# Kernel tuning notes

Measured on AMD Instinct MI355X. Metric: run time of the kernel, lower is better.

The kernel has to match this reference:

```python
import jax, jax.numpy as jnp
import numpy as np

KERNEL_MUL = 2.0
KERNEL_NUM = 5


def _pairwise_sq_dists(total):
    # ||a-b||^2 = ||a||^2 + ||b||^2 - 2 a.b  (same math as expand-subtract-square-sum)
    sq = jnp.sum(total * total, axis=1)  # [N]
    gram = total @ total.T               # [N, N]
    d2 = sq[:, None] + sq[None, :] - 2.0 * gram
    return jnp.maximum(d2, 0.0)


def setup_inputs() -> dict:
    key = jax.random.key(0)
    k1, k2 = jax.random.split(key)
    source = jax.random.normal(k1, (4096, 256), dtype=jnp.float32)
    target = jax.random.normal(k2, (4096, 256), dtype=jnp.float32)
    return {"source": source, "target": target}


def reference(source, target):
    bs = source.shape[0]
    n_samples = source.shape[0] + target.shape[0]
    total = jnp.concatenate([source, target], axis=0)  # [N, D]
    l2 = _pairwise_sq_dists(total)                      # [N, N]
    # bandwidth computed from detached distances (torch .data)
    bandwidth = jax.lax.stop_gradient(jnp.sum(l2)) / (n_samples ** 2 - n_samples)
    bandwidth = bandwidth / (KERNEL_MUL ** (KERNEL_NUM // 2))
    kernels = jnp.zeros_like(l2)
    for i in range(KERNEL_NUM):
        kernels = kernels + jnp.exp(-l2 / (bandwidth * (KERNEL_MUL ** i)))
    xx = jnp.mean(kernels[:bs, :bs])
    yy = jnp.mean(kernels[bs:, bs:])
    xy = jnp.mean(kernels[:bs, bs:])
    yx = jnp.mean(kernels[bs:, :bs])
    return xx + yy - xy - yx
```

## Files before the change

kernel.cpp:

```cpp
#include <hip/hip_runtime.h>
#include <stdint.h>
#include <stddef.h>


#define N_TOT 8192
#define D_DIM 256
#define BS    4096
#define NB    64
#define NTILE 2080

typedef float  f32x4  __attribute__((ext_vector_type(4)));
typedef short  bf16x8 __attribute__((ext_vector_type(8)));

typedef __attribute__((address_space(1))) const unsigned int gas_u32;
typedef __attribute__((address_space(3))) unsigned int       lds_u32;

__device__ __forceinline__ unsigned short f2bf(float f) {
  unsigned u = __float_as_uint(f);
  u += 0x7fffu + ((u >> 16) & 1u);
  return (unsigned short)(u >> 16);
}
__device__ __forceinline__ float bf2f(unsigned short s) {
  return __uint_as_float(((unsigned)s) << 16);
}

__global__ void prep_kernel(const float* __restrict__ src, const float* __restrict__ tgt,
                            unsigned short* __restrict__ Xbt, float* __restrict__ sq,
                            float* __restrict__ csp) {
  int tid  = threadIdx.x;
  int w    = tid >> 6, lane = tid & 63;
  int blk  = blockIdx.x;
  float4 cacc = {0.f, 0.f, 0.f, 0.f};

  #pragma unroll
  for (int r = 0; r < 4; ++r) {
    int row = blk * 32 + w * 4 + r;
    const float* rowp = (row < BS) ? (src + (size_t)row * D_DIM)
                                   : (tgt + (size_t)(row - BS) * D_DIM);
    float4 v = reinterpret_cast<const float4*>(rowp)[lane];
    cacc.x += v.x; cacc.y += v.y; cacc.z += v.z; cacc.w += v.w;
    ushort4 b;
    b.x = f2bf(v.x); b.y = f2bf(v.y); b.z = f2bf(v.z); b.w = f2bf(v.w);
    int k = lane * 4;
    size_t off = ((size_t)(row >> 4)) * 4096 + (size_t)(k >> 3) * 128
               + (size_t)((row & 15) * 8) + (k & 7);
    *reinterpret_cast<ushort4*>(Xbt + off) = b;
    float fx = bf2f(b.x), fy = bf2f(b.y), fz = bf2f(b.z), fw = bf2f(b.w);
    float s = fx * fx + fy * fy + fz * fz + fw * fw;
    #pragma unroll
    for (int o = 32; o; o >>= 1) s += __shfl_down(s, o, 64);
    if (lane == 0) sq[row] = s;
  }

  __shared__ float cs[8][256];
  reinterpret_cast<float4*>(&cs[w][0])[lane] = cacc;
  __syncthreads();
  if (tid < 256) {
    float s = 0.f;
    #pragma unroll
    for (int ww = 0; ww < 8; ++ww) s += cs[ww][tid];
    csp[blk * 256 + tid] = s;
  }
}

__global__ void bw_kernel(const float* __restrict__ sq, const float* __restrict__ csp,
                          float* __restrict__ coef) {
  int t = threadIdx.x, w = t >> 6, lane = t & 63;
  double s1 = 0.0;
  #pragma unroll
  for (int i = 0; i < 32; ++i) s1 += (double)sq[t + i * 256];
  double c = 0.0;
  #pragma unroll 16
  for (int b = 0; b < 256; ++b) c += (double)csp[b * 256 + t];
  double s2 = c * c;
  #pragma unroll
  for (int o = 32; o; o >>= 1) { s1 += __shfl_down(s1, o, 64); s2 += __shfl_down(s2, o, 64); }
  __shared__ double rs[4], rs2[4];
  if (lane == 0) { rs[w] = s1; rs2[w] = s2; }
  __syncthreads();
  if (t == 0) {
    double S1 = rs[0] + rs[1] + rs[2] + rs[3];
    double S2 = rs2[0] + rs2[1] + rs2[2] + rs2[3];
    double S  = 2.0 * (double)N_TOT * S1 - 2.0 * S2;
    double bw = (S / ((double)N_TOT * (double)N_TOT - (double)N_TOT)) / 4.0;
    *coef = (float)(-1.4426950408889634 / (16.0 * bw));
  }
}

__launch_bounds__(256, 2)
__global__ void gram_kernel(const unsigned short* __restrict__ Xbt, const float* __restrict__ sq,
                            const float* __restrict__ coefp, double* __restrict__ partial) {
  __shared__ __align__(16) unsigned char Alds[65536];

  int tid = threadIdx.x;
  int w = tid >> 6, lane = tid & 63;
  const int lo = lane & 15, hi = lane >> 4;
  const int wr = w >> 1, wc = w & 1;

  int orig = (int)blockIdx.x;
  int id   = (orig & 7) * (NTILE / 8) + (orig >> 3);

  int bi = 0, bj = 0;
  {
    int rem = id, Mi = 0, Mj = 0;
    for (Mi = 0; Mi < 8; ++Mi) {
      bool found = false;
      for (Mj = Mi; Mj < 8; ++Mj) {
        int cntm = (Mi == Mj) ? 36 : 64;
        if (rem < cntm) { found = true; break; }
        rem -= cntm;
      }
      if (found) break;
    }
    int ti, tj;
    if (Mi == Mj) {
      ti = 0;
      while (rem >= 8 - ti) { rem -= 8 - ti; ++ti; }
      tj = ti + rem;
    } else {
      ti = rem >> 3; tj = rem & 7;
    }
    bi = Mi * 8 + ti; bj = Mj * 8 + tj;
  }

  float factor = ((bi < 32) == (bj < 32)) ? 1.f : -1.f;
  if (bi != bj) factor *= 2.f;

  const char* Xb = (const char*)Xbt;

  {
    const char* srcA = Xb + (size_t)bi * 65536 + w * 16384 + lane * 16;
    unsigned char* dstA = Alds + w * 16384;
    #pragma unroll
    for (int i = 0; i < 16; ++i)
      __builtin_amdgcn_global_load_lds((gas_u32*)(srcA + i * 1024),
                                       (lds_u32*)(dstA + i * 1024), 16, 0, 0);
  }

  const char* pB = Xb + (size_t)(bj * 8 + wc * 4) * 8192 + (hi * 256 + lo * 16);
  const char* pAl = (const char*)Alds + (size_t)(wr * 4) * 8192 + (hi * 256 + lo * 16);

  f32x4 acc[4][4];
  #pragma unroll
  for (int m = 0; m < 4; ++m)
    #pragma unroll
    for (int n = 0; n < 4; ++n) acc[m][n] = (f32x4){0.f, 0.f, 0.f, 0.f};

  __syncthreads();

  #pragma unroll
  for (int kc = 0; kc < 8; ++kc) {
    bf16x8 a[4], b[4];
    #pragma unroll
    for (int n = 0; n < 4; ++n) b[n] = *(const bf16x8*)(pB + n * 8192 + kc * 1024);
    #pragma unroll
    for (int m = 0; m < 4; ++m) a[m] = *(const bf16x8*)(pAl + m * 8192 + kc * 1024);
    #pragma unroll
    for (int m = 0; m < 4; ++m)
      #pragma unroll
      for (int n = 0; n < 4; ++n)
        acc[m][n] = __builtin_amdgcn_mfma_f32_16x16x32_bf16(a[m], b[n], acc[m][n], 0, 0, 0);
  }

  float coef = *coefp;
  float sqj[4], sqi[4][4];
  #pragma unroll
  for (int n = 0; n < 4; ++n) sqj[n] = sq[bj * 128 + wc * 64 + n * 16 + lo];
  #pragma unroll
  for (int m = 0; m < 4; ++m)
    #pragma unroll
    for (int r = 0; r < 4; ++r) sqi[m][r] = sq[bi * 128 + wr * 64 + m * 16 + hi * 4 + r];

  float psum = 0.f;
  #pragma unroll
  for (int m = 0; m < 4; ++m) {
    #pragma unroll
    for (int n = 0; n < 4; ++n) {
      #pragma unroll
      for (int r = 0; r < 4; ++r) {
        float g  = acc[m][n][r];
        float d2 = fmaxf(fmaf(-2.f, g, sqi[m][r] + sqj[n]), 0.f);
        float u  = __builtin_amdgcn_exp2f(d2 * coef);
        float u2 = u * u, u4 = u2 * u2, u8 = u4 * u4, u16 = u8 * u8;
        psum += (u + u2) + (u4 + u8) + u16;
      }
    }
  }
  #pragma unroll
  for (int o = 32; o; o >>= 1) psum += __shfl_down(psum, o, 64);
  __shared__ float wred[4];
  if (lane == 0) wred[w] = psum;
  __syncthreads();
  if (tid == 0)
    partial[id] = (double)((wred[0] + wred[1] + wred[2] + wred[3]) * factor);
}

__global__ void reduce_kernel(const double* __restrict__ partial, float* __restrict__ out) {
  int t = threadIdx.x, w = t >> 6, lane = t & 63;
  double s = 0.0;
  for (int i = t; i < NTILE; i += 256) s += partial[i];
  #pragma unroll
  for (int o = 32; o; o >>= 1) s += __shfl_down(s, o, 64);
  __shared__ double rs[4];
  if (lane == 0) rs[w] = s;
  __syncthreads();
  if (t == 0)
    out[0] = (float)((rs[0] + rs[1] + rs[2] + rs[3]) / ((double)BS * (double)BS));
}

extern "C" void kernel_launch(void* const* d_in, const int* in_sizes, int n_in,
                              void* d_out, int out_size, void* d_ws, size_t ws_size,
                              hipStream_t stream) {
  const float* src = (const float*)d_in[0];
  const float* tgt = (const float*)d_in[1];
  char* ws = (char*)d_ws;
  float*  coef    = (float*)(ws + 0);
  double* partial = (double*)(ws + 64);
  float*  csp     = (float*)(ws + 16704);
  float*  sq      = (float*)(ws + 278848);
  unsigned short* Xbt = (unsigned short*)(ws + 311616);
  float* out = (float*)d_out;

  prep_kernel<<<256, 512, 0, stream>>>(src, tgt, Xbt, sq, csp);
  bw_kernel<<<1, 256, 0, stream>>>(sq, csp, coef);
  gram_kernel<<<NTILE, 256, 0, stream>>>(Xbt, sq, coef, partial);
  reduce_kernel<<<1, 256, 0, stream>>>(partial, out);
}
```

Baseline: 58.77 us.

## Process four consecutive upper-triangle tiles per block, reusing staged A rows

Each gram block now walks four consecutive tiles in row-major upper-triangle order instead of one tile from a blocked 8x8 super-tile ordering. The LDS copy of the A row block is restaged only when the tile row changes, so most tiles skip the 64KB global-to-LDS load. The goal is less A staging traffic and fewer block launches. The cost is a 4x smaller grid (520 blocks), which limits parallelism and latency hiding, and a loss of the previous L2-friendly super-tile ordering for B reads.

```diff
diff --git a/kernel.cpp b/kernel.cpp
--- a/kernel.cpp
+++ b/kernel.cpp
@@ -8,6 +8,7 @@
 #define BS    4096
 #define NB    64
 #define NTILE 2080
+#define NBLK  520
 
 typedef float  f32x4  __attribute__((ext_vector_type(4)));
 typedef short  bf16x8 __attribute__((ext_vector_type(8)));
@@ -98,107 +99,99 @@
   const int wr = w >> 1, wc = w & 1;
 
   int orig = (int)blockIdx.x;
-  int id   = (orig & 7) * (NTILE / 8) + (orig >> 3);
-
-  int bi = 0, bj = 0;
-  {
-    int rem = id, Mi = 0, Mj = 0;
-    for (Mi = 0; Mi < 8; ++Mi) {
-      bool found = false;
-      for (Mj = Mi; Mj < 8; ++Mj) {
-        int cntm = (Mi == Mj) ? 36 : 64;
-        if (rem < cntm) { found = true; break; }
-        rem -= cntm;
-      }
-      if (found) break;
+  int blk  = (orig & 7) * (NBLK / 8) + (orig >> 3);
+  int id   = blk * 4;
+
+  int bi = 0, rem = id;
+  while (rem >= NB - bi) { rem -= NB - bi; ++bi; }
+  int bj = bi + rem;
+
+  const char* Xb = (const char*)Xbt;
+  float coef = *coefp;
+  int bi_staged = -1;
+  double dsum = 0.0;
+
+  for (int t = 0; t < 4; ++t) {
+    if (bi != bi_staged) {
+      __syncthreads();
+      const char* srcA = Xb + (size_t)bi * 65536 + w * 16384 + lane * 16;
+      unsigned char* dstA = Alds + w * 16384;
+      #pragma unroll
+      for (int i = 0; i < 16; ++i)
+        __builtin_amdgcn_global_load_lds((gas_u32*)(srcA + i * 1024),
+                                         (lds_u32*)(dstA + i * 1024), 16, 0, 0);
+      __syncthreads();
+      bi_staged = bi;
     }
-    int ti, tj;
-    if (Mi == Mj) {
-      ti = 0;
-      while (rem >= 8 - ti) { rem -= 8 - ti; ++ti; }
-      tj = ti + rem;
-    } else {
-      ti = rem >> 3; tj = rem & 7;
+
+    float factor = ((bi < 32) == (bj < 32)) ? 1.f : -1.f;
+    if (bi != bj) factor *= 2.f;
+
+    const char* pB  = Xb + (size_t)(bj * 8 + wc * 4) * 8192 + (hi * 256 + lo * 16);
+    const char* pAl = (const char*)Alds + (size_t)(wr * 4) * 8192 + (hi * 256 + lo * 16);
+
+    f32x4 acc[4][4];
+    #pragma unroll
+    for (int m = 0; m < 4; ++m)
+      #pragma unroll
+      for (int n = 0; n < 4; ++n) acc[m][n] = (f32x4){0.f, 0.f, 0.f, 0.f};
+
+    #pragma unroll
+    for (int kc = 0; kc < 8; ++kc) {
+      bf16x8 a[4], b[4];
+      #pragma unroll
+      for (int n = 0; n < 4; ++n) b[n] = *(const bf16x8*)(pB + n * 8192 + kc * 1024);
+      #pragma unroll
+      for (int m = 0; m < 4; ++m) a[m] = *(const bf16x8*)(pAl + m * 8192 + kc * 1024);
+      #pragma unroll
+      for (int m = 0; m < 4; ++m)
+        #pragma unroll
+        for (int n = 0; n < 4; ++n)
+          acc[m][n] = __builtin_amdgcn_mfma_f32_16x16x32_bf16(a[m], b[n], acc[m][n], 0, 0, 0);
     }
-    bi = Mi * 8 + ti; bj = Mj * 8 + tj;
-  }
-
-  float factor = ((bi < 32) == (bj < 32)) ? 1.f : -1.f;
-  if (bi != bj) factor *= 2.f;
-
-  const char* Xb = (const char*)Xbt;
-
-  {
-    const char* srcA = Xb + (size_t)bi * 65536 + w * 16384 + lane * 16;
-    unsigned char* dstA = Alds + w * 16384;
-    #pragma unroll
-    for (int i = 0; i < 16; ++i)
-      __builtin_amdgcn_global_load_lds((gas_u32*)(srcA + i * 1024),
-                                       (lds_u32*)(dstA + i * 1024), 16, 0, 0);
-  }
-
-  const char* pB = Xb + (size_t)(bj * 8 + wc * 4) * 8192 + (hi * 256 + lo * 16);
-  const char* pAl = (const char*)Alds + (size_t)(wr * 4) * 8192 + (hi * 256 + lo * 16);
-
-  f32x4 acc[4][4];
-  #pragma unroll
-  for (int m = 0; m < 4; ++m)
-    #pragma unroll
-    for (int n = 0; n < 4; ++n) acc[m][n] = (f32x4){0.f, 0.f, 0.f, 0.f};
-
-  __syncthreads();
-
-  #pragma unroll
-  for (int kc = 0; kc < 8; ++kc) {
-    bf16x8 a[4], b[4];
-    #pragma unroll
-    for (int n = 0; n < 4; ++n) b[n] = *(const bf16x8*)(pB + n * 8192 + kc * 1024);
-    #pragma unroll
-    for (int m = 0; m < 4; ++m) a[m] = *(const bf16x8*)(pAl + m * 8192 + kc * 1024);
+
+    float sqj[4], sqi[4][4];
+    #pragma unroll
+    for (int n = 0; n < 4; ++n) sqj[n] = sq[bj * 128 + wc * 64 + n * 16 + lo];
     #pragma unroll
     for (int m = 0; m < 4; ++m)
       #pragma unroll
-      for (int n = 0; n < 4; ++n)
-        acc[m][n] = __builtin_amdgcn_mfma_f32_16x16x32_bf16(a[m], b[n], acc[m][n], 0, 0, 0);
-  }
-
-  float coef = *coefp;
-  float sqj[4], sqi[4][4];
-  #pragma unroll
-  for (int n = 0; n < 4; ++n) sqj[n] = sq[bj * 128 + wc * 64 + n * 16 + lo];
-  #pragma unroll
-  for (int m = 0; m < 4; ++m)
-    #pragma unroll
-    for (int r = 0; r < 4; ++r) sqi[m][r] = sq[bi * 128 + wr * 64 + m * 16 + hi * 4 + r];
-
-  float psum = 0.f;
-  #pragma unroll
-  for (int m = 0; m < 4; ++m) {
-    #pragma unroll
-    for (int n = 0; n < 4; ++n) {
-      #pragma unroll
-      for (int r = 0; r < 4; ++r) {
-        float g  = acc[m][n][r];
-        float d2 = fmaxf(fmaf(-2.f, g, sqi[m][r] + sqj[n]), 0.f);
-        float u  = __builtin_amdgcn_exp2f(d2 * coef);
-        float u2 = u * u, u4 = u2 * u2, u8 = u4 * u4, u16 = u8 * u8;
-        psum += (u + u2) + (u4 + u8) + u16;
+      for (int r = 0; r < 4; ++r) sqi[m][r] = sq[bi * 128 + wr * 64 + m * 16 + hi * 4 + r];
+
+    float psum = 0.f;
+    #pragma unroll
+    for (int m = 0; m < 4; ++m) {
+      #pragma unroll
+      for (int n = 0; n < 4; ++n) {
+        #pragma unroll
+        for (int r = 0; r < 4; ++r) {
+          float g  = acc[m][n][r];
+          float d2 = fmaxf(fmaf(-2.f, g, sqi[m][r] + sqj[n]), 0.f);
+          float u  = __builtin_amdgcn_exp2f(d2 * coef);
+          float u2 = u * u, u4 = u2 * u2, u8 = u4 * u4, u16 = u8 * u8;
+          psum += (u + u2) + (u4 + u8) + u16;
+        }
       }
     }
-  }
-  #pragma unroll
-  for (int o = 32; o; o >>= 1) psum += __shfl_down(psum, o, 64);
-  __shared__ float wred[4];
-  if (lane == 0) wred[w] = psum;
+    #pragma unroll
+    for (int o = 32; o; o >>= 1) psum += __shfl_down(psum, o, 64);
+    if (lane == 0) dsum += (double)(psum * factor);
+
+    ++bj;
+    if (bj == NB) { ++bi; bj = bi; }
+  }
+
+  __shared__ double wred[4];
+  if (lane == 0) wred[w] = dsum;
   __syncthreads();
   if (tid == 0)
-    partial[id] = (double)((wred[0] + wred[1] + wred[2] + wred[3]) * factor);
+    partial[blk] = wred[0] + wred[1] + wred[2] + wred[3];
 }
 
 __global__ void reduce_kernel(const double* __restrict__ partial, float* __restrict__ out) {
   int t = threadIdx.x, w = t >> 6, lane = t & 63;
   double s = 0.0;
-  for (int i = t; i < NTILE; i += 256) s += partial[i];
+  for (int i = t; i < NBLK; i += 256) s += partial[i];
   #pragma unroll
   for (int o = 32; o; o >>= 1) s += __shfl_down(s, o, 64);
   __shared__ double rs[4];
@@ -223,6 +216,6 @@
 
   prep_kernel<<<256, 512, 0, stream>>>(src, tgt, Xbt, sq, csp);
   bw_kernel<<<1, 256, 0, stream>>>(sq, csp, coef);
-  gram_kernel<<<NTILE, 256, 0, stream>>>(Xbt, sq, coef, partial);
+  gram_kernel<<<NBLK, 256, 0, stream>>>(Xbt, sq, coef, partial);
   reduce_kernel<<<1, 256, 0, stream>>>(partial, out);
 }
```

Measured after the change: 62.63 us. +6.6%, slower.

## Retile Gram kernel into 64x256 tiles with 8 waves and register-pipelined loads

Applied to the files above, without the earlier changes.

Replaces the 128x128 upper-triangular tiling with 64-row by 256-column tiles across 8 waves. Each block stages a smaller A panel in LDS while the B fragments are loaded straight into registers. K-loop loads are double-buffered for A and prefetched four steps ahead for B, and diagonal-straddling tiles use a per-element weight mask instead of a per-tile factor. This aims to raise occupancy and overlap loads with MFMA, at the cost of some redundant work on the tiles below the diagonal and extra per-element compare logic.

```diff
diff --git a/kernel.cpp b/kernel.cpp
--- a/kernel.cpp
+++ b/kernel.cpp
@@ -6,8 +6,7 @@
 #define N_TOT 8192
 #define D_DIM 256
 #define BS    4096
-#define NB    64
-#define NTILE 2080
+#define NTILE 2112
 
 typedef float  f32x4  __attribute__((ext_vector_type(4)));
 typedef short  bf16x8 __attribute__((ext_vector_type(8)));
@@ -87,112 +86,125 @@
   }
 }
 
-__launch_bounds__(256, 2)
+__launch_bounds__(512, 4)
 __global__ void gram_kernel(const unsigned short* __restrict__ Xbt, const float* __restrict__ sq,
                             const float* __restrict__ coefp, double* __restrict__ partial) {
-  __shared__ __align__(16) unsigned char Alds[65536];
+  __shared__ __align__(16) unsigned char Alds[32768];
 
   int tid = threadIdx.x;
   int w = tid >> 6, lane = tid & 63;
   const int lo = lane & 15, hi = lane >> 4;
-  const int wr = w >> 1, wc = w & 1;
+  const int fragoff = hi * 256 + lo * 16;
 
   int orig = (int)blockIdx.x;
-  int id   = (orig & 7) * (NTILE / 8) + (orig >> 3);
-
-  int bi = 0, bj = 0;
+  int blk  = (orig & 7) * (NTILE / 8) + (orig >> 3);
+
+  int i, j;
   {
-    int rem = id, Mi = 0, Mj = 0;
-    for (Mi = 0; Mi < 8; ++Mi) {
-      bool found = false;
-      for (Mj = Mi; Mj < 8; ++Mj) {
-        int cntm = (Mi == Mj) ? 36 : 64;
-        if (rem < cntm) { found = true; break; }
-        rem -= cntm;
-      }
-      if (found) break;
-    }
-    int ti, tj;
-    if (Mi == Mj) {
-      ti = 0;
-      while (rem >= 8 - ti) { rem -= 8 - ti; ++ti; }
-      tj = ti + rem;
-    } else {
-      ti = rem >> 3; tj = rem & 7;
-    }
-    bi = Mi * 8 + ti; bj = Mj * 8 + tj;
-  }
-
-  float factor = ((bi < 32) == (bj < 32)) ? 1.f : -1.f;
-  if (bi != bj) factor *= 2.f;
+    int rem = blk, q = 0;
+    while (rem >= 4 * (32 - q)) { rem -= 4 * (32 - q); ++q; }
+    int per = 32 - q;
+    i = q * 4 + rem / per;
+    j = q + rem % per;
+  }
+
+  float sgn = ((i < 64) == (j < 16)) ? 1.f : -1.f;
 
   const char* Xb = (const char*)Xbt;
 
+  const char* pB0 = Xb + (size_t)(j * 16 + 2 * w) * 8192 + fragoff;
+  const char* pB1 = pB0 + 8192;
+
+  bf16x8 b[4][2], a[2][4];
+  #pragma unroll
+  for (int s = 0; s < 4; ++s) {
+    b[s][0] = *(const bf16x8*)(pB0 + s * 1024);
+    b[s][1] = *(const bf16x8*)(pB1 + s * 1024);
+  }
+
   {
-    const char* srcA = Xb + (size_t)bi * 65536 + w * 16384 + lane * 16;
-    unsigned char* dstA = Alds + w * 16384;
-    #pragma unroll
-    for (int i = 0; i < 16; ++i)
-      __builtin_amdgcn_global_load_lds((gas_u32*)(srcA + i * 1024),
-                                       (lds_u32*)(dstA + i * 1024), 16, 0, 0);
-  }
-
-  const char* pB = Xb + (size_t)(bj * 8 + wc * 4) * 8192 + (hi * 256 + lo * 16);
-  const char* pAl = (const char*)Alds + (size_t)(wr * 4) * 8192 + (hi * 256 + lo * 16);
-
-  f32x4 acc[4][4];
+    const char* srcA = Xb + (size_t)i * 32768 + w * 4096 + lane * 16;
+    unsigned char* dstA = Alds + w * 4096;
+    #pragma unroll
+    for (int q2 = 0; q2 < 4; ++q2)
+      __builtin_amdgcn_global_load_lds((gas_u32*)(srcA + q2 * 1024),
+                                       (lds_u32*)(dstA + q2 * 1024), 16, 0, 0);
+  }
+  __syncthreads();
+
+  const char* pAl = (const char*)Alds + fragoff;
+
+  f32x4 acc[4][2];
+  #pragma unroll
+  for (int m = 0; m < 4; ++m) {
+    acc[m][0] = (f32x4){0.f, 0.f, 0.f, 0.f};
+    acc[m][1] = (f32x4){0.f, 0.f, 0.f, 0.f};
+  }
+
+  #pragma unroll
+  for (int m = 0; m < 4; ++m) a[0][m] = *(const bf16x8*)(pAl + m * 8192);
+
+  #pragma unroll
+  for (int kc = 0; kc < 8; ++kc) {
+    if (kc + 1 < 8) {
+      #pragma unroll
+      for (int m = 0; m < 4; ++m)
+        a[(kc + 1) & 1][m] = *(const bf16x8*)(pAl + m * 8192 + (kc + 1) * 1024);
+    }
+    #pragma unroll
+    for (int m = 0; m < 4; ++m) {
+      acc[m][0] = __builtin_amdgcn_mfma_f32_16x16x32_bf16(a[kc & 1][m], b[kc & 3][0],
+                                                          acc[m][0], 0, 0, 0);
+      acc[m][1] = __builtin_amdgcn_mfma_f32_16x16x32_bf16(a[kc & 1][m], b[kc & 3][1],
+                                                          acc[m][1], 0, 0, 0);
+    }
+    if (kc + 4 < 8) {
+      b[kc & 3][0] = *(const bf16x8*)(pB0 + (kc + 4) * 1024);
+      b[kc & 3][1] = *(const bf16x8*)(pB1 + (kc + 4) * 1024);
+    }
+  }
+
+  float coef = *coefp;
+  int rowbase = i * 64;
+  int colbase = j * 256 + w * 32;
+  float sqj[2], sqi[4][4];
+  #pragma unroll
+  for (int n = 0; n < 2; ++n) sqj[n] = sq[colbase + n * 16 + lo];
   #pragma unroll
   for (int m = 0; m < 4; ++m)
     #pragma unroll
-    for (int n = 0; n < 4; ++n) acc[m][n] = (f32x4){0.f, 0.f, 0.f, 0.f};
-
-  __syncthreads();
-
-  #pragma unroll
-  for (int kc = 0; kc < 8; ++kc) {
-    bf16x8 a[4], b[4];
-    #pragma unroll
-    for (int n = 0; n < 4; ++n) b[n] = *(const bf16x8*)(pB + n * 8192 + kc * 1024);
-    #pragma unroll
-    for (int m = 0; m < 4; ++m) a[m] = *(const bf16x8*)(pAl + m * 8192 + kc * 1024);
-    #pragma unroll
-    for (int m = 0; m < 4; ++m)
-      #pragma unroll
-      for (int n = 0; n < 4; ++n)
-        acc[m][n] = __builtin_amdgcn_mfma_f32_16x16x32_bf16(a[m], b[n], acc[m][n], 0, 0, 0);
-  }
-
-  float coef = *coefp;
-  float sqj[4], sqi[4][4];
-  #pragma unroll
-  for (int n = 0; n < 4; ++n) sqj[n] = sq[bj * 128 + wc * 64 + n * 16 + lo];
-  #pragma unroll
-  for (int m = 0; m < 4; ++m)
-    #pragma unroll
-    for (int r = 0; r < 4; ++r) sqi[m][r] = sq[bi * 128 + wr * 64 + m * 16 + hi * 4 + r];
+    for (int r = 0; r < 4; ++r) sqi[m][r] = sq[rowbase + m * 16 + hi * 4 + r];
 
   float psum = 0.f;
   #pragma unroll
   for (int m = 0; m < 4; ++m) {
     #pragma unroll
-    for (int n = 0; n < 4; ++n) {
+    for (int n = 0; n < 2; ++n) {
+      int col = colbase + n * 16 + lo;
       #pragma unroll
       for (int r = 0; r < 4; ++r) {
+        int row = rowbase + m * 16 + hi * 4 + r;
+        float wgt = (col > row) ? 2.f : ((col == row) ? 1.f : 0.f);
         float g  = acc[m][n][r];
         float d2 = fmaxf(fmaf(-2.f, g, sqi[m][r] + sqj[n]), 0.f);
         float u  = __builtin_amdgcn_exp2f(d2 * coef);
         float u2 = u * u, u4 = u2 * u2, u8 = u4 * u4, u16 = u8 * u8;
-        psum += (u + u2) + (u4 + u8) + u16;
+        psum += wgt * ((u + u2) + (u4 + u8) + u16);
       }
     }
   }
   #pragma unroll
   for (int o = 32; o; o >>= 1) psum += __shfl_down(psum, o, 64);
-  __shared__ float wred[4];
+
+  __shared__ float wred[8];
   if (lane == 0) wred[w] = psum;
   __syncthreads();
-  if (tid == 0)
-    partial[id] = (double)((wred[0] + wred[1] + wred[2] + wred[3]) * factor);
+  if (tid == 0) {
+    float s = 0.f;
+    #pragma unroll
+    for (int ww = 0; ww < 8; ++ww) s += wred[ww];
+    partial[blk] = (double)(s * sgn);
+  }
 }
 
 __global__ void reduce_kernel(const double* __restrict__ partial, float* __restrict__ out) {
@@ -216,13 +228,13 @@
   char* ws = (char*)d_ws;
   float*  coef    = (float*)(ws + 0);
   double* partial = (double*)(ws + 64);
-  float*  csp     = (float*)(ws + 16704);
-  float*  sq      = (float*)(ws + 278848);
-  unsigned short* Xbt = (unsigned short*)(ws + 311616);
+  float*  csp     = (float*)(ws + 20480);
+  float*  sq      = (float*)(ws + 282624);
+  unsigned short* Xbt = (unsigned short*)(ws + 315392);
   float* out = (float*)d_out;
 
   prep_kernel<<<256, 512, 0, stream>>>(src, tgt, Xbt, sq, csp);
   bw_kernel<<<1, 256, 0, stream>>>(sq, csp, coef);
-  gram_kernel<<<NTILE, 256, 0, stream>>>(Xbt, sq, coef, partial);
+  gram_kernel<<<NTILE, 512, 0, stream>>>(Xbt, sq, coef, partial);
   reduce_kernel<<<1, 256, 0, stream>>>(partial, out);
 }
```

Measured after the change: 59.22 us. Within noise of the previous version (+0.8%).
